# Performance work log

Measured on AMD Instinct MI355X. Metric: run time of the kernel, lower is better.

## Reference

```python
import jax, jax.numpy as jnp
import numpy as np

# Module config (matches init_kwargs); num_heads must be 1 for the original
# torch code to type-check (score_proj: Linear(d_model, num_heads) applied to
# a head_dim-sized last axis, then squeeze(-1)).
B, S, D, H = 4, 512, 256, 1
DH = D // H  # head_dim == d_model when H == 1


def _linear_init(k, out_f, in_f):
    bound = 1.0 / np.sqrt(in_f)
    kw, kb = jax.random.split(k)
    W = jax.random.uniform(kw, (out_f, in_f), jnp.float32, -bound, bound)
    b = jax.random.uniform(kb, (out_f,), jnp.float32, -bound, bound)
    return W, b


def setup_inputs() -> dict:
    key = jax.random.key(0)
    ks = jax.random.split(key, 8)
    Wq, bq = _linear_init(ks[3], D, D)
    Wk, bk = _linear_init(ks[4], D, D)
    Wv, bv = _linear_init(ks[5], D, D)
    Ws, bs = _linear_init(ks[6], H, D)   # score_proj: d_model -> num_heads
    Wo, bo = _linear_init(ks[7], D, D)
    return {
        "query": jax.random.normal(ks[0], (B, S, D), jnp.float32),
        "key": jax.random.normal(ks[1], (B, S, D), jnp.float32),
        "value": jax.random.normal(ks[2], (B, S, D), jnp.float32),
        "Wq": Wq, "bq": bq, "Wk": Wk, "bk": bk, "Wv": Wv, "bv": bv,
        "Ws": Ws, "bs": bs, "Wo": Wo, "bo": bo,
    }


def reference(query, key, value, Wq, bq, Wk, bk, Wv, bv, Ws, bs, Wo, bo):
    b, s, _ = query.shape
    # Projections, split into heads: (B, H, S, DH)
    q = (query @ Wq.T + bq).reshape(b, s, H, DH).transpose(0, 2, 1, 3)
    k = (key @ Wk.T + bk).reshape(b, s, H, DH).transpose(0, 2, 1, 3)
    v = (value @ Wv.T + bv).reshape(b, s, H, DH).transpose(0, 2, 1, 3)
    # Bahdanau additive scores: tanh of pairwise sum -> (B, H, Sq, Sk, DH)
    t = jnp.tanh(q[:, :, :, None, :] + k[:, :, None, :, :])
    # score_proj (out_features == 1 when H == 1), then squeeze(-1)
    scores = jnp.einsum('bhqkd,od->bhqko', t, Ws) + bs  # (B,H,Sq,Sk,1)
    scores = scores[..., 0]                              # (B,H,Sq,Sk)
    attn = jax.nn.softmax(scores, axis=-1)
    # Weighted sum of values, merge heads back: (B, S, D)
    attended = jnp.einsum('bhqk,bhkd->bqhd', attn, v).reshape(b, s, D)
    out = attended @ Wo.T + bo  # dropout p=0.0 (eval) -> identity
    return out, attn
```

## Files before the change

kernel.cpp:

```cpp
#include <hip/hip_runtime.h>

typedef __attribute__((ext_vector_type(8))) short short8;
typedef __attribute__((ext_vector_type(4))) float f32x4;

constexpr int BATCH = 4;
constexpr int SEQ   = 512;
constexpr int DM    = 256;

#define MFMA(a,b,c) __builtin_amdgcn_mfma_f32_16x16x32_bf16((a),(b),(c),0,0,0)

__device__ __forceinline__ unsigned short bf16h(float x) {
    unsigned u = __float_as_uint(x);
    return (unsigned short)((u + 0x7FFF + ((u >> 16) & 1)) >> 16);
}
__device__ __forceinline__ float bf16f(unsigned short h) {
    return __uint_as_float(((unsigned)h) << 16);
}
__device__ __forceinline__ float exp2x_clamped(float x) {
    x = fminf(5.0f, fmaxf(-5.0f, x));
    return __builtin_amdgcn_exp2f(x * 2.8853900817779268f);
}
__device__ __forceinline__ void cvt8(const float* s, int4& h, int4& l) {
    unsigned hw[8], lw[8];
    #pragma unroll
    for (int j = 0; j < 8; ++j) {
        unsigned short hb = bf16h(s[j]);
        hw[j] = hb;
        lw[j] = bf16h(s[j] - bf16f(hb));
    }
    h.x = (int)(hw[0] | (hw[1] << 16)); h.y = (int)(hw[2] | (hw[3] << 16));
    h.z = (int)(hw[4] | (hw[5] << 16)); h.w = (int)(hw[6] | (hw[7] << 16));
    l.x = (int)(lw[0] | (lw[1] << 16)); l.y = (int)(lw[2] | (lw[3] << 16));
    l.z = (int)(lw[4] | (lw[5] << 16)); l.w = (int)(lw[6] | (lw[7] << 16));
}

__global__ __launch_bounds__(256) void conv_kernel(
    const float* __restrict__ q, const float* __restrict__ k, const float* __restrict__ v,
    const float* __restrict__ Wq, const float* __restrict__ Wk,
    const float* __restrict__ Wv, const float* __restrict__ Wo,
    ushort* qh, ushort* ql, ushort* kh, ushort* kl, ushort* vh, ushort* vl,
    ushort* Wqh, ushort* Wql, ushort* Wkh, ushort* Wkl,
    ushort* Wvh, ushort* Wvl, ushort* Woh, ushort* Wol)
{
    const float* s; ushort* h; ushort* l; int n;
    switch (blockIdx.y) {
        case 0: s = q;  h = qh;  l = ql;  n = 524288; break;
        case 1: s = k;  h = kh;  l = kl;  n = 524288; break;
        case 2: s = v;  h = vh;  l = vl;  n = 524288; break;
        case 3: s = Wq; h = Wqh; l = Wql; n = 65536;  break;
        case 4: s = Wk; h = Wkh; l = Wkl; n = 65536;  break;
        case 5: s = Wv; h = Wvh; l = Wvl; n = 65536;  break;
        default:s = Wo; h = Woh; l = Wol; n = 65536;  break;
    }
    int idx = (blockIdx.x * 256 + threadIdx.x) * 8;
    if (idx >= n) return;
    float4 f0 = *(const float4*)(s + idx);
    float4 f1 = *(const float4*)(s + idx + 4);
    float xs[8] = {f0.x, f0.y, f0.z, f0.w, f1.x, f1.y, f1.z, f1.w};
    int4 ph, pl;
    cvt8(xs, ph, pl);
    *(int4*)&h[idx] = ph;
    *(int4*)&l[idx] = pl;
}

template<int EPI, int ASRC>
__device__ __forceinline__ void mfma_core(
    const ushort* __restrict__ Ah, const ushort* __restrict__ Al,
    const float*  __restrict__ A0, const float*  __restrict__ A1, long ldA,
    const ushort* __restrict__ Bh, const ushort* __restrict__ Bl, long ldB,
    float* __restrict__ C, long ldC, const float* __restrict__ bias,
    ushort* __restrict__ Th, ushort* __restrict__ Tl, long ldT)
{
    __shared__ short lds[16384];
    const int tid = threadIdx.x;
    const int i0 = tid, i1 = tid + 256;
    const int r0 = ((i0 >> 7) << 4) | (i0 & 15), r1 = ((i1 >> 7) << 4) | (i1 & 15);
    const int c0 = ((i0 >> 4) & 7) * 8,          c1 = ((i1 >> 4) & 7) * 8;
    const long a0o = (long)r0 * ldA + c0, a1o = (long)r1 * ldA + c1;
    const long b0o = (long)r0 * ldB + c0, b1o = (long)r1 * ldB + c1;

    int4 rah0, rah1, ral0, ral1, rbh0, rbh1, rbl0, rbl1;
    float4 fa00, fa01, fa10, fa11, ga00, ga01, ga10, ga11;

    auto issue_loads = [&](int it) {
        long off = (long)it * 64;
        if constexpr (ASRC == 2) {
            fa00 = *(const float4*)(A0 + a0o + off); fa01 = *(const float4*)(A0 + a0o + off + 4);
            fa10 = *(const float4*)(A0 + a1o + off); fa11 = *(const float4*)(A0 + a1o + off + 4);
            ga00 = *(const float4*)(A1 + a0o + off); ga01 = *(const float4*)(A1 + a0o + off + 4);
            ga10 = *(const float4*)(A1 + a1o + off); ga11 = *(const float4*)(A1 + a1o + off + 4);
        } else {
            rah0 = *(const int4*)(Ah + a0o + off); rah1 = *(const int4*)(Ah + a1o + off);
            ral0 = *(const int4*)(Al + a0o + off); ral1 = *(const int4*)(Al + a1o + off);
        }
        rbh0 = *(const int4*)(Bh + b0o + off); rbh1 = *(const int4*)(Bh + b1o + off);
        rbl0 = *(const int4*)(Bl + b0o + off); rbl1 = *(const int4*)(Bl + b1o + off);
    };
    auto write_lds = [&]() {
        if constexpr (ASRC == 2) {
            float s0[8] = {fa00.x+ga00.x, fa00.y+ga00.y, fa00.z+ga00.z, fa00.w+ga00.w,
                           fa01.x+ga01.x, fa01.y+ga01.y, fa01.z+ga01.z, fa01.w+ga01.w};
            float s1[8] = {fa10.x+ga10.x, fa10.y+ga10.y, fa10.z+ga10.z, fa10.w+ga10.w,
                           fa11.x+ga11.x, fa11.y+ga11.y, fa11.z+ga11.z, fa11.w+ga11.w};
            int4 h, l2;
            cvt8(s0, h, l2);
            *(int4*)&lds[i0 * 8] = h; *(int4*)&lds[4096 + i0 * 8] = l2;
            cvt8(s1, h, l2);
            *(int4*)&lds[i1 * 8] = h; *(int4*)&lds[4096 + i1 * 8] = l2;
        } else {
            *(int4*)&lds[i0 * 8] = rah0;        *(int4*)&lds[i1 * 8] = rah1;
            *(int4*)&lds[4096 + i0 * 8] = ral0; *(int4*)&lds[4096 + i1 * 8] = ral1;
        }
        *(int4*)&lds[8192  + i0 * 8] = rbh0; *(int4*)&lds[8192  + i1 * 8] = rbh1;
        *(int4*)&lds[12288 + i0 * 8] = rbl0; *(int4*)&lds[12288 + i1 * 8] = rbl1;
    };

    const int l = tid & 63, w = tid >> 6;
    const int ms = (w >> 1) * 2, ns = (w & 1) * 2;
    f32x4 acc00 = {0,0,0,0}, acc01 = {0,0,0,0}, acc10 = {0,0,0,0}, acc11 = {0,0,0,0};

    issue_loads(0);
    for (int it = 0; it < 4; ++it) {
        write_lds();
        __syncthreads();
        if (it < 3) issue_loads(it + 1);
        const int lo = l * 8;
        #pragma unroll
        for (int ks = 0; ks < 2; ++ks) {
            short8 a0h = *(const short8*)&lds[((ms    ) * 2 + ks) * 512 + lo];
            short8 a1h = *(const short8*)&lds[((ms + 1) * 2 + ks) * 512 + lo];
            short8 a0l = *(const short8*)&lds[4096 + ((ms    ) * 2 + ks) * 512 + lo];
            short8 a1l = *(const short8*)&lds[4096 + ((ms + 1) * 2 + ks) * 512 + lo];
            short8 b0h = *(const short8*)&lds[8192 + ((ns    ) * 2 + ks) * 512 + lo];
            short8 b1h = *(const short8*)&lds[8192 + ((ns + 1) * 2 + ks) * 512 + lo];
            short8 b0l = *(const short8*)&lds[12288 + ((ns    ) * 2 + ks) * 512 + lo];
            short8 b1l = *(const short8*)&lds[12288 + ((ns + 1) * 2 + ks) * 512 + lo];
            acc00 = MFMA(a0h, b0h, acc00); acc00 = MFMA(a0h, b0l, acc00); acc00 = MFMA(a0l, b0h, acc00);
            acc01 = MFMA(a0h, b1h, acc01); acc01 = MFMA(a0h, b1l, acc01); acc01 = MFMA(a0l, b1h, acc01);
            acc10 = MFMA(a1h, b0h, acc10); acc10 = MFMA(a1h, b0l, acc10); acc10 = MFMA(a1l, b0h, acc10);
            acc11 = MFMA(a1h, b1h, acc11); acc11 = MFMA(a1h, b1l, acc11); acc11 = MFMA(a1l, b1h, acc11);
        }
        __syncthreads();
    }

    auto epi = [&](int i, int j, f32x4 a) {
        const int n  = (ns + j) * 16 + (l & 15);
        const int mb = (ms + i) * 16 + (l >> 4) * 4;
        if constexpr (EPI == 1) {
            float bb = bias[n];
            float x0 = a.x + bb, x1 = a.y + bb, x2 = a.z + bb, x3 = a.w + bb;
            unsigned short h0 = bf16h(x0), h1 = bf16h(x1), h2 = bf16h(x2), h3 = bf16h(x3);
            int2 ph, pl;
            ph.x = (int)(h0 | ((unsigned)h1 << 16));
            ph.y = (int)(h2 | ((unsigned)h3 << 16));
            pl.x = (int)(bf16h(x0 - bf16f(h0)) | ((unsigned)bf16h(x1 - bf16f(h1)) << 16));
            pl.y = (int)(bf16h(x2 - bf16f(h2)) | ((unsigned)bf16h(x3 - bf16f(h3)) << 16));
            *(int2*)&Th[(long)n * ldT + mb] = ph;
            *(int2*)&Tl[(long)n * ldT + mb] = pl;
        } else {
            float bb = bias[n];
            float xs[4] = {a.x, a.y, a.z, a.w};
            #pragma unroll
            for (int r = 0; r < 4; ++r) {
                float x = xs[r] + bb;
                if constexpr (EPI == 0) x = exp2x_clamped(x);
                C[(long)(mb + r) * ldC + n] = x;
            }
        }
    };
    epi(0, 0, acc00); epi(0, 1, acc01); epi(1, 0, acc10); epi(1, 1, acc11);
}

__global__ __launch_bounds__(256) void proj_mfma(
    const ushort* qh, const ushort* ql, const ushort* kh, const ushort* kl,
    const ushort* vh, const ushort* vl,
    const ushort* Wqh, const ushort* Wql, const ushort* Wkh, const ushort* Wkl,
    const ushort* Wvh, const ushort* Wvl,
    const float* bq, const float* bk, const float* bv,
    float* Eq, float* Ek, ushort* vpTh, ushort* vpTl)
{
    const int z = blockIdx.z;
    const long m0 = blockIdx.x * 64, n0 = blockIdx.y * 64;
    const ushort *Ah, *Al, *Bh, *Bl; const float* bias;
    if (z == 0)      { Ah = qh; Al = ql; Bh = Wqh; Bl = Wql; bias = bq; }
    else if (z == 1) { Ah = kh; Al = kl; Bh = Wkh; Bl = Wkl; bias = bk; }
    else             { Ah = vh; Al = vl; Bh = Wvh; Bl = Wvl; bias = bv; }
    Ah += m0 * 256; Al += m0 * 256; Bh += n0 * 256; Bl += n0 * 256; bias += n0;
    if (z < 2) {
        float* C = (z ? Ek : Eq) + m0 * 256 + n0;
        mfma_core<0, 0>(Ah, Al, nullptr, nullptr, 256, Bh, Bl, 256,
                        C, 256, bias, nullptr, nullptr, 0);
    } else {
        mfma_core<1, 0>(Ah, Al, nullptr, nullptr, 256, Bh, Bl, 256,
                        nullptr, 0, bias,
                        vpTh + n0 * 2048 + m0, vpTl + n0 * 2048 + m0, 2048);
    }
}

__global__ __launch_bounds__(256) void scores_kernel(
    const float* __restrict__ Eq, const float* __restrict__ Ek,
    const float* __restrict__ Ws, float* __restrict__ part)
{
    __shared__ __align__(16) float qL[64][68];
    __shared__ __align__(16) float kL[64][68];
    const int z = blockIdx.z;
    const int b = z >> 1, c = z & 1;
    const int q0 = blockIdx.x * 64, k0 = blockIdx.y * 64;
    const int tid = threadIdx.x;
    const int qi = tid >> 4, ki = tid & 15;

    float acc[4][4] = {};
    for (int cc = 0; cc < 2; ++cc) {
        const int c0 = c * 128 + cc * 64;
        const float* Eqb = Eq + ((long)b * SEQ + q0) * DM + c0;
        const float* Ekb = Ek + ((long)b * SEQ + k0) * DM + c0;
        if (cc) __syncthreads();
        #pragma unroll
        for (int i = 0; i < 4; ++i) {
            int f = i * 256 + tid;
            int r = f >> 4, col = (f & 15) << 2;
            *(float4*)&qL[r][col] = *(const float4*)(Eqb + (long)r * DM + col);
            *(float4*)&kL[r][col] = *(const float4*)(Ekb + (long)r * DM + col);
        }
        __syncthreads();
        #pragma unroll 2
        for (int d = 0; d < 64; d += 4) {
            float4 w4 = *(const float4*)(Ws + c0 + d);
            float4 av[4], bv[4];
            #pragma unroll
            for (int i = 0; i < 4; ++i) av[i] = *(const float4*)&qL[qi + 16 * i][d];
            #pragma unroll
            for (int j = 0; j < 4; ++j) bv[j] = *(const float4*)&kL[ki + 16 * j][d];
            #pragma unroll
            for (int i = 0; i < 4; ++i)
                #pragma unroll
                for (int j = 0; j < 4; ++j) {
                    float xp = fmaf(av[i].x, bv[j].x, 1.0f);
                    float yp = fmaf(av[i].y, bv[j].y, 1.0f);
                    float zp = fmaf(av[i].z, bv[j].z, 1.0f);
                    float wp = fmaf(av[i].w, bv[j].w, 1.0f);
                    float xy = xp * yp, zw = zp * wp;
                    float n1 = fmaf(w4.x, yp, w4.y * xp);
                    float n2 = fmaf(w4.z, wp, w4.w * zp);
                    float num = fmaf(n1, zw, n2 * xy);
                    acc[i][j] = fmaf(num, __builtin_amdgcn_rcpf(xy * zw), acc[i][j]);
                }
        }
    }

    float* pb = part + (long)c * (BATCH * SEQ * SEQ) + (long)b * SEQ * SEQ;
    #pragma unroll
    for (int i = 0; i < 4; ++i) {
        float* row = pb + (long)(q0 + qi + 16 * i) * SEQ + k0 + ki;
        #pragma unroll
        for (int j = 0; j < 4; ++j) row[16 * j] = acc[i][j];
    }
}

__global__ __launch_bounds__(256) void attnv_fused(
    const float* __restrict__ part,
    const ushort* __restrict__ vpTh, const ushort* __restrict__ vpTl,
    float* __restrict__ attn, float* __restrict__ att0, float* __restrict__ att1)
{
    __shared__ short lds[16384];
    __shared__ float inv[64];
    const int z = blockIdx.z, b = z >> 1, h = z & 1;
    const long m0 = blockIdx.x * 64, n0 = blockIdx.y * 64;
    const int tid = threadIdx.x;
    constexpr long PS = (long)BATCH * SEQ * SEQ;
    constexpr float NL2E = -2.0f * 1.4426950408889634f;

    {
        const int r = tid >> 2, qn = tid & 3;
        const float* p0 = part + ((long)b * SEQ + m0 + r) * SEQ + qn * 128;
        const float* p1 = p0 + PS;
        float s = 0.f;
        #pragma unroll 8
        for (int j = 0; j < 128; j += 4) {
            float4 a = *(const float4*)(p0 + j);
            float4 c = *(const float4*)(p1 + j);
            s += __builtin_amdgcn_exp2f(NL2E * (a.x + c.x));
            s += __builtin_amdgcn_exp2f(NL2E * (a.y + c.y));
            s += __builtin_amdgcn_exp2f(NL2E * (a.z + c.z));
            s += __builtin_amdgcn_exp2f(NL2E * (a.w + c.w));
        }
        s += __shfl_xor(s, 1);
        s += __shfl_xor(s, 2);
        if (qn == 0) inv[r] = __builtin_amdgcn_rcpf(s);
    }
    __syncthreads();

    const int i0 = tid, i1 = tid + 256;
    const int r0 = ((i0 >> 7) << 4) | (i0 & 15), r1 = ((i1 >> 7) << 4) | (i1 & 15);
    const int c0 = ((i0 >> 4) & 7) * 8,          c1 = ((i1 >> 4) & 7) * 8;

    const ushort* Bh = vpTh + n0 * 2048 + (long)b * SEQ + h * 256;
    const ushort* Bl = vpTl + n0 * 2048 + (long)b * SEQ + h * 256;
    const long b0o = (long)r0 * 2048 + c0, b1o = (long)r1 * 2048 + c1;

    const float* pA = part + ((long)b * SEQ + m0) * SEQ + h * 256;
    float* attnW = (blockIdx.y == 0)
        ? attn + ((long)b * SEQ + m0) * SEQ + h * 256 : nullptr;

    int4 rbh0, rbh1, rbl0, rbl1;
    float e0[8], e1[8];

    auto issue = [&](int it) {
        long off = (long)it * 64;
        const float* q0p = pA + (long)r0 * SEQ + off + c0;
        const float* q1p = pA + (long)r1 * SEQ + off + c1;
        float4 x0 = *(const float4*)(q0p),      x1 = *(const float4*)(q0p + 4);
        float4 y0 = *(const float4*)(q0p + PS), y1 = *(const float4*)(q0p + PS + 4);
        float4 u0 = *(const float4*)(q1p),      u1 = *(const float4*)(q1p + 4);
        float4 v0 = *(const float4*)(q1p + PS), v1 = *(const float4*)(q1p + PS + 4);
        e0[0] = __builtin_amdgcn_exp2f(NL2E * (x0.x + y0.x));
        e0[1] = __builtin_amdgcn_exp2f(NL2E * (x0.y + y0.y));
        e0[2] = __builtin_amdgcn_exp2f(NL2E * (x0.z + y0.z));
        e0[3] = __builtin_amdgcn_exp2f(NL2E * (x0.w + y0.w));
        e0[4] = __builtin_amdgcn_exp2f(NL2E * (x1.x + y1.x));
        e0[5] = __builtin_amdgcn_exp2f(NL2E * (x1.y + y1.y));
        e0[6] = __builtin_amdgcn_exp2f(NL2E * (x1.z + y1.z));
        e0[7] = __builtin_amdgcn_exp2f(NL2E * (x1.w + y1.w));
        e1[0] = __builtin_amdgcn_exp2f(NL2E * (u0.x + v0.x));
        e1[1] = __builtin_amdgcn_exp2f(NL2E * (u0.y + v0.y));
        e1[2] = __builtin_amdgcn_exp2f(NL2E * (u0.z + v0.z));
        e1[3] = __builtin_amdgcn_exp2f(NL2E * (u0.w + v0.w));
        e1[4] = __builtin_amdgcn_exp2f(NL2E * (u1.x + v1.x));
        e1[5] = __builtin_amdgcn_exp2f(NL2E * (u1.y + v1.y));
        e1[6] = __builtin_amdgcn_exp2f(NL2E * (u1.z + v1.z));
        e1[7] = __builtin_amdgcn_exp2f(NL2E * (u1.w + v1.w));
        rbh0 = *(const int4*)(Bh + b0o + off); rbh1 = *(const int4*)(Bh + b1o + off);
        rbl0 = *(const int4*)(Bl + b0o + off); rbl1 = *(const int4*)(Bl + b1o + off);
    };
    auto writeL = [&](int it) {
        int4 hh, ll;
        cvt8(e0, hh, ll);
        *(int4*)&lds[i0 * 8] = hh; *(int4*)&lds[4096 + i0 * 8] = ll;
        cvt8(e1, hh, ll);
        *(int4*)&lds[i1 * 8] = hh; *(int4*)&lds[4096 + i1 * 8] = ll;
        *(int4*)&lds[8192  + i0 * 8] = rbh0; *(int4*)&lds[8192  + i1 * 8] = rbh1;
        *(int4*)&lds[12288 + i0 * 8] = rbl0; *(int4*)&lds[12288 + i1 * 8] = rbl1;
        if (attnW) {
            long off = (long)it * 64;
            float iv0 = inv[r0], iv1 = inv[r1];
            float* w0 = attnW + (long)r0 * SEQ + off + c0;
            float* w1 = attnW + (long)r1 * SEQ + off + c1;
            float4 o;
            o.x = e0[0]*iv0; o.y = e0[1]*iv0; o.z = e0[2]*iv0; o.w = e0[3]*iv0;
            *(float4*)w0 = o;
            o.x = e0[4]*iv0; o.y = e0[5]*iv0; o.z = e0[6]*iv0; o.w = e0[7]*iv0;
            *(float4*)(w0 + 4) = o;
            o.x = e1[0]*iv1; o.y = e1[1]*iv1; o.z = e1[2]*iv1; o.w = e1[3]*iv1;
            *(float4*)w1 = o;
            o.x = e1[4]*iv1; o.y = e1[5]*iv1; o.z = e1[6]*iv1; o.w = e1[7]*iv1;
            *(float4*)(w1 + 4) = o;
        }
    };

    const int l = tid & 63, w = tid >> 6;
    const int ms = (w >> 1) * 2, ns = (w & 1) * 2;
    f32x4 acc00 = {0,0,0,0}, acc01 = {0,0,0,0}, acc10 = {0,0,0,0}, acc11 = {0,0,0,0};

    issue(0);
    for (int it = 0; it < 4; ++it) {
        writeL(it);
        __syncthreads();
        if (it < 3) issue(it + 1);
        const int lo = l * 8;
        #pragma unroll
        for (int ks = 0; ks < 2; ++ks) {
            short8 a0h = *(const short8*)&lds[((ms    ) * 2 + ks) * 512 + lo];
            short8 a1h = *(const short8*)&lds[((ms + 1) * 2 + ks) * 512 + lo];
            short8 a0l = *(const short8*)&lds[4096 + ((ms    ) * 2 + ks) * 512 + lo];
            short8 a1l = *(const short8*)&lds[4096 + ((ms + 1) * 2 + ks) * 512 + lo];
            short8 b0h = *(const short8*)&lds[8192 + ((ns    ) * 2 + ks) * 512 + lo];
            short8 b1h = *(const short8*)&lds[8192 + ((ns + 1) * 2 + ks) * 512 + lo];
            short8 b0l = *(const short8*)&lds[12288 + ((ns    ) * 2 + ks) * 512 + lo];
            short8 b1l = *(const short8*)&lds[12288 + ((ns + 1) * 2 + ks) * 512 + lo];
            acc00 = MFMA(a0h, b0h, acc00); acc00 = MFMA(a0h, b0l, acc00); acc00 = MFMA(a0l, b0h, acc00);
            acc01 = MFMA(a0h, b1h, acc01); acc01 = MFMA(a0h, b1l, acc01); acc01 = MFMA(a0l, b1h, acc01);
            acc10 = MFMA(a1h, b0h, acc10); acc10 = MFMA(a1h, b0l, acc10); acc10 = MFMA(a1l, b0h, acc10);
            acc11 = MFMA(a1h, b1h, acc11); acc11 = MFMA(a1h, b1l, acc11); acc11 = MFMA(a1l, b1h, acc11);
        }
        __syncthreads();
    }

    float* Cp = (h ? att1 : att0) + ((long)b * SEQ + m0) * DM + n0;
    auto epi = [&](int i, int j, f32x4 a) {
        const int n  = (ns + j) * 16 + (l & 15);
        const int mb = (ms + i) * 16 + (l >> 4) * 4;
        float xs[4] = {a.x, a.y, a.z, a.w};
        #pragma unroll
        for (int r = 0; r < 4; ++r)
            Cp[(long)(mb + r) * DM + n] = xs[r] * inv[mb + r];
    };
    epi(0, 0, acc00); epi(0, 1, acc01); epi(1, 0, acc10); epi(1, 1, acc11);
}

__global__ __launch_bounds__(256) void out_mfma(
    const float* att0, const float* att1,
    const ushort* Woh, const ushort* Wol, const float* bo, float* out)
{
    const long m0 = blockIdx.x * 64, n0 = blockIdx.y * 64;
    mfma_core<2, 2>(nullptr, nullptr, att0 + m0 * 256, att1 + m0 * 256, 256,
                    Woh + n0 * 256, Wol + n0 * 256, 256,
                    out + m0 * 256 + n0, 256, bo + n0, nullptr, nullptr, 0);
}

extern "C" void kernel_launch(void* const* d_in, const int* in_sizes, int n_in,
                              void* d_out, int out_size, void* d_ws, size_t ws_size,
                              hipStream_t stream) {
    const float* query = (const float*)d_in[0];
    const float* key   = (const float*)d_in[1];
    const float* value = (const float*)d_in[2];
    const float* Wq = (const float*)d_in[3];
    const float* bq = (const float*)d_in[4];
    const float* Wk = (const float*)d_in[5];
    const float* bk = (const float*)d_in[6];
    const float* Wv = (const float*)d_in[7];
    const float* bv = (const float*)d_in[8];
    const float* Ws = (const float*)d_in[9];
    const float* Wo = (const float*)d_in[11];
    const float* bo = (const float*)d_in[12];

    float* out  = (float*)d_out;
    float* attn = (float*)d_out + (long)BATCH * SEQ * DM;

    float* ws = (float*)d_ws;
    float* Eq   = ws;
    float* Ek   = ws + 524288;
    float* part = ws + 1048576;
    float* att0 = ws + 3145728;
    float* att1 = ws + 3670016;
    ushort* u = (ushort*)(ws + 4194304);
    ushort* qh  = u;              ushort* ql  = qh  + 524288;
    ushort* kh  = ql  + 524288;   ushort* kl  = kh  + 524288;
    ushort* vh  = kl  + 524288;   ushort* vl  = vh  + 524288;
    ushort* Wqh = vl  + 524288;   ushort* Wql = Wqh + 65536;
    ushort* Wkh = Wql + 65536;    ushort* Wkl = Wkh + 65536;
    ushort* Wvh = Wkl + 65536;    ushort* Wvl = Wvh + 65536;
    ushort* Woh = Wvl + 65536;    ushort* Wol = Woh + 65536;
    ushort* vpTh = Wol + 65536;   ushort* vpTl = vpTh + 524288;

    conv_kernel  <<<dim3(256, 7),   256, 0, stream>>>(query, key, value, Wq, Wk, Wv, Wo,
                                                      qh, ql, kh, kl, vh, vl,
                                                      Wqh, Wql, Wkh, Wkl, Wvh, Wvl, Woh, Wol);
    proj_mfma    <<<dim3(32, 4, 3), 256, 0, stream>>>(qh, ql, kh, kl, vh, vl,
                                                      Wqh, Wql, Wkh, Wkl, Wvh, Wvl,
                                                      bq, bk, bv, Eq, Ek, vpTh, vpTl);
    scores_kernel<<<dim3(8, 8, 8),  256, 0, stream>>>(Eq, Ek, Ws, part);
    attnv_fused  <<<dim3(8, 4, 8),  256, 0, stream>>>(part, vpTh, vpTl, attn, att0, att1);
    out_mfma     <<<dim3(32, 4),    256, 0, stream>>>(att0, att1, Woh, Wol, bo, out);
}
```

Before: 76.08 us.

## Fuse exp and row-sum into scores kernel, drop split-D partial buffers

```diff
diff --git a/kernel.cpp b/kernel.cpp
--- a/kernel.cpp
+++ b/kernel.cpp
@@ -40,8 +40,14 @@
     const float* __restrict__ Wv, const float* __restrict__ Wo,
     ushort* qh, ushort* ql, ushort* kh, ushort* kl, ushort* vh, ushort* vl,
     ushort* Wqh, ushort* Wql, ushort* Wkh, ushort* Wkl,
-    ushort* Wvh, ushort* Wvl, ushort* Woh, ushort* Wol)
-{
+    ushort* Wvh, ushort* Wvl, ushort* Woh, ushort* Wol,
+    float* rowsum)
+{
+    if (blockIdx.y == 7) {
+        int idx = blockIdx.x * 256 + threadIdx.x;
+        if (idx < BATCH * SEQ) rowsum[idx] = 0.f;
+        return;
+    }
     const float* s; ushort* h; ushort* l; int n;
     switch (blockIdx.y) {
         case 0: s = q;  h = qh;  l = ql;  n = 524288; break;
@@ -199,19 +205,19 @@
 
 __global__ __launch_bounds__(256) void scores_kernel(
     const float* __restrict__ Eq, const float* __restrict__ Ek,
-    const float* __restrict__ Ws, float* __restrict__ part)
+    const float* __restrict__ Ws, float* __restrict__ e_out,
+    float* __restrict__ rowsum)
 {
     __shared__ __align__(16) float qL[64][68];
     __shared__ __align__(16) float kL[64][68];
-    const int z = blockIdx.z;
-    const int b = z >> 1, c = z & 1;
+    const int b = blockIdx.z;
     const int q0 = blockIdx.x * 64, k0 = blockIdx.y * 64;
     const int tid = threadIdx.x;
     const int qi = tid >> 4, ki = tid & 15;
 
     float acc[4][4] = {};
-    for (int cc = 0; cc < 2; ++cc) {
-        const int c0 = c * 128 + cc * 64;
+    for (int cc = 0; cc < 4; ++cc) {
+        const int c0 = cc * 64;
         const float* Eqb = Eq + ((long)b * SEQ + q0) * DM + c0;
         const float* Ekb = Ek + ((long)b * SEQ + k0) * DM + c0;
         if (cc) __syncthreads();
@@ -248,7 +254,28 @@
         }
     }
 
-    float* pb = part + (long)c * (BATCH * SEQ * SEQ) + (long)b * SEQ * SEQ;
+    constexpr float NL2E = -2.0f * 1.4426950408889634f;
+    float rs[4];
+    #pragma unroll
+    for (int i = 0; i < 4; ++i) {
+        float s = 0.f;
+        #pragma unroll
+        for (int j = 0; j < 4; ++j) {
+            float e = __builtin_amdgcn_exp2f(NL2E * acc[i][j]);
+            acc[i][j] = e;
+            s += e;
+        }
+        s += __shfl_xor(s, 1); s += __shfl_xor(s, 2);
+        s += __shfl_xor(s, 4); s += __shfl_xor(s, 8);
+        rs[i] = s;
+    }
+    if (ki == 0) {
+        #pragma unroll
+        for (int i = 0; i < 4; ++i)
+            atomicAdd(&rowsum[(long)b * SEQ + q0 + qi + 16 * i], rs[i]);
+    }
+
+    float* pb = e_out + (long)b * SEQ * SEQ;
     #pragma unroll
     for (int i = 0; i < 4; ++i) {
         float* row = pb + (long)(q0 + qi + 16 * i) * SEQ + k0 + ki;
@@ -258,7 +285,7 @@
 }
 
 __global__ __launch_bounds__(256) void attnv_fused(
-    const float* __restrict__ part,
+    const float* __restrict__ e_in, const float* __restrict__ rowsum,
     const ushort* __restrict__ vpTh, const ushort* __restrict__ vpTl,
     float* __restrict__ attn, float* __restrict__ att0, float* __restrict__ att1)
 {
@@ -267,27 +294,9 @@
     const int z = blockIdx.z, b = z >> 1, h = z & 1;
     const long m0 = blockIdx.x * 64, n0 = blockIdx.y * 64;
     const int tid = threadIdx.x;
-    constexpr long PS = (long)BATCH * SEQ * SEQ;
-    constexpr float NL2E = -2.0f * 1.4426950408889634f;
-
-    {
-        const int r = tid >> 2, qn = tid & 3;
-        const float* p0 = part + ((long)b * SEQ + m0 + r) * SEQ + qn * 128;
-        const float* p1 = p0 + PS;
-        float s = 0.f;
-        #pragma unroll 8
-        for (int j = 0; j < 128; j += 4) {
-            float4 a = *(const float4*)(p0 + j);
-            float4 c = *(const float4*)(p1 + j);
-            s += __builtin_amdgcn_exp2f(NL2E * (a.x + c.x));
-            s += __builtin_amdgcn_exp2f(NL2E * (a.y + c.y));
-            s += __builtin_amdgcn_exp2f(NL2E * (a.z + c.z));
-            s += __builtin_amdgcn_exp2f(NL2E * (a.w + c.w));
-        }
-        s += __shfl_xor(s, 1);
-        s += __shfl_xor(s, 2);
-        if (qn == 0) inv[r] = __builtin_amdgcn_rcpf(s);
-    }
+
+    if (tid < 64)
+        inv[tid] = __builtin_amdgcn_rcpf(rowsum[(long)b * SEQ + m0 + tid]);
     __syncthreads();
 
     const int i0 = tid, i1 = tid + 256;
@@ -298,7 +307,7 @@
     const ushort* Bl = vpTl + n0 * 2048 + (long)b * SEQ + h * 256;
     const long b0o = (long)r0 * 2048 + c0, b1o = (long)r1 * 2048 + c1;
 
-    const float* pA = part + ((long)b * SEQ + m0) * SEQ + h * 256;
+    const float* pA = e_in + ((long)b * SEQ + m0) * SEQ + h * 256;
     float* attnW = (blockIdx.y == 0)
         ? attn + ((long)b * SEQ + m0) * SEQ + h * 256 : nullptr;
 
@@ -309,26 +318,12 @@
         long off = (long)it * 64;
         const float* q0p = pA + (long)r0 * SEQ + off + c0;
         const float* q1p = pA + (long)r1 * SEQ + off + c1;
-        float4 x0 = *(const float4*)(q0p),      x1 = *(const float4*)(q0p + 4);
-        float4 y0 = *(const float4*)(q0p + PS), y1 = *(const float4*)(q0p + PS + 4);
-        float4 u0 = *(const float4*)(q1p),      u1 = *(const float4*)(q1p + 4);
-        float4 v0 = *(const float4*)(q1p + PS), v1 = *(const float4*)(q1p + PS + 4);
-        e0[0] = __builtin_amdgcn_exp2f(NL2E * (x0.x + y0.x));
-        e0[1] = __builtin_amdgcn_exp2f(NL2E * (x0.y + y0.y));
-        e0[2] = __builtin_amdgcn_exp2f(NL2E * (x0.z + y0.z));
-        e0[3] = __builtin_amdgcn_exp2f(NL2E * (x0.w + y0.w));
-        e0[4] = __builtin_amdgcn_exp2f(NL2E * (x1.x + y1.x));
-        e0[5] = __builtin_amdgcn_exp2f(NL2E * (x1.y + y1.y));
-        e0[6] = __builtin_amdgcn_exp2f(NL2E * (x1.z + y1.z));
-        e0[7] = __builtin_amdgcn_exp2f(NL2E * (x1.w + y1.w));
-        e1[0] = __builtin_amdgcn_exp2f(NL2E * (u0.x + v0.x));
-        e1[1] = __builtin_amdgcn_exp2f(NL2E * (u0.y + v0.y));
-        e1[2] = __builtin_amdgcn_exp2f(NL2E * (u0.z + v0.z));
-        e1[3] = __builtin_amdgcn_exp2f(NL2E * (u0.w + v0.w));
-        e1[4] = __builtin_amdgcn_exp2f(NL2E * (u1.x + v1.x));
-        e1[5] = __builtin_amdgcn_exp2f(NL2E * (u1.y + v1.y));
-        e1[6] = __builtin_amdgcn_exp2f(NL2E * (u1.z + v1.z));
-        e1[7] = __builtin_amdgcn_exp2f(NL2E * (u1.w + v1.w));
+        float4 x0 = *(const float4*)(q0p), x1 = *(const float4*)(q0p + 4);
+        float4 u0 = *(const float4*)(q1p), u1 = *(const float4*)(q1p + 4);
+        e0[0] = x0.x; e0[1] = x0.y; e0[2] = x0.z; e0[3] = x0.w;
+        e0[4] = x1.x; e0[5] = x1.y; e0[6] = x1.z; e0[7] = x1.w;
+        e1[0] = u0.x; e1[1] = u0.y; e1[2] = u0.z; e1[3] = u0.w;
+        e1[4] = u1.x; e1[5] = u1.y; e1[6] = u1.z; e1[7] = u1.w;
         rbh0 = *(const int4*)(Bh + b0o + off); rbh1 = *(const int4*)(Bh + b1o + off);
         rbl0 = *(const int4*)(Bl + b0o + off); rbl1 = *(const int4*)(Bl + b1o + off);
     };
@@ -427,12 +422,13 @@
     float* attn = (float*)d_out + (long)BATCH * SEQ * DM;
 
     float* ws = (float*)d_ws;
-    float* Eq   = ws;
-    float* Ek   = ws + 524288;
-    float* part = ws + 1048576;
-    float* att0 = ws + 3145728;
-    float* att1 = ws + 3670016;
-    ushort* u = (ushort*)(ws + 4194304);
+    float* Eq     = ws;
+    float* Ek     = ws + 524288;
+    float* e_buf  = ws + 1048576;
+    float* att0   = ws + 2097152;
+    float* att1   = ws + 2621440;
+    float* rowsum = ws + 3145728;
+    ushort* u = (ushort*)(ws + 3147776);
     ushort* qh  = u;              ushort* ql  = qh  + 524288;
     ushort* kh  = ql  + 524288;   ushort* kl  = kh  + 524288;
     ushort* vh  = kl  + 524288;   ushort* vl  = vh  + 524288;
@@ -442,13 +438,15 @@
     ushort* Woh = Wvl + 65536;    ushort* Wol = Woh + 65536;
     ushort* vpTh = Wol + 65536;   ushort* vpTl = vpTh + 524288;
 
-    conv_kernel  <<<dim3(256, 7),   256, 0, stream>>>(query, key, value, Wq, Wk, Wv, Wo,
+    conv_kernel  <<<dim3(256, 8),   256, 0, stream>>>(query, key, value, Wq, Wk, Wv, Wo,
                                                       qh, ql, kh, kl, vh, vl,
-                                                      Wqh, Wql, Wkh, Wkl, Wvh, Wvl, Woh, Wol);
+                                                      Wqh, Wql, Wkh, Wkl, Wvh, Wvl, Woh, Wol,
+                                                      rowsum);
     proj_mfma    <<<dim3(32, 4, 3), 256, 0, stream>>>(qh, ql, kh, kl, vh, vl,
                                                       Wqh, Wql, Wkh, Wkl, Wvh, Wvl,
                                                       bq, bk, bv, Eq, Ek, vpTh, vpTl);
-    scores_kernel<<<dim3(8, 8, 8),  256, 0, stream>>>(Eq, Ek, Ws, part);
-    attnv_fused  <<<dim3(8, 4, 8),  256, 0, stream>>>(part, vpTh, vpTl, attn, att0, att1);
+    scores_kernel<<<dim3(8, 8, 4),  256, 0, stream>>>(Eq, Ek, Ws, e_buf, rowsum);
+    attnv_fused  <<<dim3(8, 4, 8),  256, 0, stream>>>(e_buf, rowsum, vpTh, vpTl,
+                                                      attn, att0, att1);
     out_mfma     <<<dim3(32, 4),    256, 0, stream>>>(att0, att1, Woh, Wol, bo, out);
 }
```

New measurement: 73.85 us. -2.9%, faster.
